# Optimization experiments

Measured on AMD Instinct MI355X. Metric: run time of the kernel, lower is better.

## Reference

```python
import jax, jax.numpy as jnp
import numpy as np

B, L, D_MODEL, H, D_K, D_V, C = 4, 2048, 512, 8, 64, 64, 5
LN_EPS = 1e-5


def setup_inputs() -> dict:
    key = jax.random.key(0)
    ks = jax.random.split(key, 9)
    u_k = min(int(C * np.log(L)), L)  # 38
    s = 1.0 / np.sqrt(D_MODEL)
    return {
        "input_Q": jax.random.normal(ks[0], (B, L, D_MODEL), jnp.float32),
        "input_K": jax.random.normal(ks[1], (B, L, D_MODEL), jnp.float32),
        "input_V": jax.random.normal(ks[2], (B, L, D_MODEL), jnp.float32),
        "W_Q": jax.random.normal(ks[3], (D_MODEL, H * D_K), jnp.float32) * s,
        "W_K": jax.random.normal(ks[4], (D_MODEL, H * D_K), jnp.float32) * s,
        "W_V": jax.random.normal(ks[5], (D_MODEL, H * D_V), jnp.float32) * s,
        "W_fc": jax.random.normal(ks[6], (H * D_V, D_MODEL), jnp.float32) * (1.0 / np.sqrt(H * D_V)),
        "ln_gamma": jnp.ones((D_MODEL,), jnp.float32),
        "ln_beta": jnp.zeros((D_MODEL,), jnp.float32),
        "index_sample": jax.random.randint(ks[7], (L, u_k), 0, L, jnp.int32),
    }


def reference(input_Q, input_K, input_V, W_Q, W_K, W_V, W_fc, ln_gamma, ln_beta, index_sample):
    Bb, L_Q, _ = input_Q.shape
    L_K = input_K.shape[1]
    u_q = min(int(C * np.log(L_Q)), L_Q)  # n_top queries kept

    # projections -> (B, H, L, d)
    Q = (input_Q @ W_Q).reshape(Bb, L_Q, H, D_K).transpose(0, 2, 1, 3)
    K = (input_K @ W_K).reshape(Bb, L_K, H, D_K).transpose(0, 2, 1, 3)
    V = (input_V @ W_V).reshape(Bb, L_K, H, D_V).transpose(0, 2, 1, 3)

    # sampled QK scores: gather u_k random keys per query position
    K_sample = K[:, :, index_sample, :]                      # (B,H,L_Q,u_k,d_k)
    QK_sample = jnp.einsum('bhqe,bhqke->bhqk', Q, K_sample)  # (B,H,L_Q,u_k)

    # sparsity measure M = max - mean, top-u_q queries
    M = QK_sample.max(axis=-1) - QK_sample.mean(axis=-1)     # (B,H,L_Q)
    _, idx = jax.lax.top_k(M, u_q)                           # (B,H,u_q)

    # attention only for selected queries
    Q_sel = jnp.take_along_axis(Q, idx[..., None], axis=2)   # (B,H,u_q,d_k)
    scores = jnp.einsum('bhue,bhke->bhuk', Q_sel, K) / np.sqrt(D_K)
    attn = jax.nn.softmax(scores, axis=-1)
    values = jnp.einsum('bhuk,bhkd->bhud', attn, V)          # (B,H,u_q,d_v)

    # initial context = mean of V (attn_mask is None), scatter selected rows
    context = jnp.broadcast_to(V.mean(axis=2, keepdims=True), (Bb, H, L_Q, D_V))
    bb = jnp.arange(Bb)[:, None, None]
    hh = jnp.arange(H)[None, :, None]
    context = context.at[bb, hh, idx].set(values)

    context = context.transpose(0, 2, 1, 3).reshape(Bb, L_Q, H * D_V)
    out = context @ W_fc                                     # dropout p=0.0

    y = out + input_Q
    mu = y.mean(axis=-1, keepdims=True)
    var = jnp.mean(jnp.square(y - mu), axis=-1, keepdims=True)
    y = (y - mu) / jnp.sqrt(var + LN_EPS) * ln_gamma + ln_beta
    return y, idx
```

## Files before the change

kernel.cpp:

```cpp
#include <hip/hip_runtime.h>
#include <hip/hip_bf16.h>

#define NB 4
#define NL 2048
#define NH 8
#define NDM 512
#define ND 64
#define KSPLIT 8
#define QB 8

typedef __attribute__((ext_vector_type(8))) short short8b;
typedef __attribute__((ext_vector_type(4))) float f32x4;

__global__ void wconv(const float* __restrict__ W, unsigned short* __restrict__ WT) {
  const int g = blockIdx.x * 256 + threadIdx.x;
  const int k = g >> 9, c = g & 511;
  __hip_bfloat16 hb = __float2bfloat16(W[(size_t)k * 512 + c]);
  WT[(size_t)c * 512 + k] = *reinterpret_cast<unsigned short*>(&hb);
}

__global__ void vmean_colmean(const float* __restrict__ inV, float* __restrict__ parts) {
  const int b = blockIdx.x, seg = blockIdx.y, t = threadIdx.x;
  const float* p = inV + ((size_t)b * NL + seg * 32) * NDM;
  float s0 = 0.f, s1 = 0.f;
  for (int r = 0; r < 32; ++r) {
    s0 += p[(size_t)r * NDM + t];
    s1 += p[(size_t)r * NDM + 256 + t];
  }
  parts[((size_t)b * 64 + seg) * NDM + t] = s0;
  parts[((size_t)b * 64 + seg) * NDM + 256 + t] = s1;
}
__global__ void vmean_gemm(const float* __restrict__ parts, const float* __restrict__ Wv,
                           float* __restrict__ Vm) {
  __shared__ float cm[512];
  const int b = blockIdx.x, t = threadIdx.x;
  float a0 = 0.f, a1 = 0.f;
  for (int g = 0; g < 64; ++g) {
    a0 += parts[((size_t)b * 64 + g) * NDM + t];
    a1 += parts[((size_t)b * 64 + g) * NDM + 256 + t];
  }
  cm[t] = a0 * (1.f / 2048.f);
  cm[t + 256] = a1 * (1.f / 2048.f);
  __syncthreads();
  const int c0 = blockIdx.y * 256 + t;
  float acc = 0.f;
  for (int k = 0; k < 512; ++k) acc += cm[k] * Wv[(size_t)k * NDM + c0];
  Vm[b * 512 + c0] = acc;
}

__global__ __launch_bounds__(256, 4) void proj3(
    const float* __restrict__ AQ, const float* __restrict__ AK,
    const float* __restrict__ wQm, const float* __restrict__ wKm,
    int gh0, float* __restrict__ Qc, float* __restrict__ Kc) {
  __shared__ float As_[32 * 132];
  __shared__ float Ws_[32 * 68];
  const int tid = threadIdx.x;
  const int bm = blockIdx.x;
  const int hl = blockIdx.y;
  const int mat = blockIdx.z;
  const int bh = gh0 + hl;
  const int b = bh >> 3, h = bh & 7;
  const float* A = (mat == 0) ? AQ : AK;
  const float* W = (mat == 0) ? wQm : wKm;
  float* D = (mat == 0) ? Qc : Kc;
  const float* Ab = A + (size_t)b * NL * NDM;
  const int colbase = h * 64;
  const int tm = tid >> 4, tn = tid & 15;
  float acc[8][4] = {};
  for (int k0 = 0; k0 < 512; k0 += 32) {
#pragma unroll
    for (int i = 0; i < 4; ++i) {
      int s = tid + i * 256;
      int r = s >> 3, c4 = (s & 7) * 4;
      float4 v = *reinterpret_cast<const float4*>(Ab + (size_t)(bm * 128 + r) * 512 + k0 + c4);
      As_[(c4 + 0) * 132 + r] = v.x;
      As_[(c4 + 1) * 132 + r] = v.y;
      As_[(c4 + 2) * 132 + r] = v.z;
      As_[(c4 + 3) * 132 + r] = v.w;
    }
#pragma unroll
    for (int i = 0; i < 2; ++i) {
      int s = tid + i * 256;
      int r = s >> 4, c4 = (s & 15) * 4;
      *reinterpret_cast<float4*>(&Ws_[r * 68 + c4]) =
          *reinterpret_cast<const float4*>(W + (size_t)(k0 + r) * 512 + colbase + c4);
    }
    __syncthreads();
#pragma unroll
    for (int kk = 0; kk < 32; ++kk) {
      float4 a0 = *reinterpret_cast<const float4*>(&As_[kk * 132 + tm * 4]);
      float4 a1 = *reinterpret_cast<const float4*>(&As_[kk * 132 + 64 + tm * 4]);
      float4 w  = *reinterpret_cast<const float4*>(&Ws_[kk * 68 + tn * 4]);
      float a[8] = {a0.x, a0.y, a0.z, a0.w, a1.x, a1.y, a1.z, a1.w};
      float wv[4] = {w.x, w.y, w.z, w.w};
#pragma unroll
      for (int ii = 0; ii < 8; ++ii)
#pragma unroll
        for (int jj = 0; jj < 4; ++jj) acc[ii][jj] += a[ii] * wv[jj];
    }
    __syncthreads();
  }
#pragma unroll
  for (int ii = 0; ii < 8; ++ii) {
    int row = bm * 128 + ((ii < 4) ? (tm * 4 + ii) : (64 + tm * 4 + (ii - 4)));
    float4 v = make_float4(acc[ii][0], acc[ii][1], acc[ii][2], acc[ii][3]);
    *reinterpret_cast<float4*>(D + ((size_t)hl * NL + row) * ND + tn * 4) = v;
  }
}

__global__ __launch_bounds__(256) void projV_mfma(
    const float* __restrict__ AV, const unsigned short* __restrict__ WT,
    int gh0, float* __restrict__ Vc) {
  const int wv = threadIdx.x >> 6, l = threadIdx.x & 63;
  const int bm = blockIdx.x;
  const int hl = blockIdx.y;
  const int bh = gh0 + hl;
  const int b = bh >> 3, h = bh & 7;
  const float* Ab = AV + (size_t)b * NL * NDM;
  const int row = bm * 64 + wv * 16 + (l & 15);
  const int kg = (l >> 4) * 8;
  f32x4 acc0 = {}, acc1 = {}, acc2 = {}, acc3 = {};
  for (int k0 = 0; k0 < 512; k0 += 32) {
    const float* ap = Ab + (size_t)row * 512 + k0 + kg;
    short8b af;
#pragma unroll
    for (int j = 0; j < 8; ++j) {
      __hip_bfloat16 hb = __float2bfloat16(ap[j]);
      af[j] = *reinterpret_cast<short*>(&hb);
    }
    const unsigned short* wp = WT + (size_t)(h * 64 + (l & 15)) * 512 + k0 + kg;
    short8b b0 = *reinterpret_cast<const short8b*>(wp);
    short8b b1 = *reinterpret_cast<const short8b*>(wp + 16 * 512);
    short8b b2 = *reinterpret_cast<const short8b*>(wp + 32 * 512);
    short8b b3 = *reinterpret_cast<const short8b*>(wp + 48 * 512);
    acc0 = __builtin_amdgcn_mfma_f32_16x16x32_bf16(af, b0, acc0, 0, 0, 0);
    acc1 = __builtin_amdgcn_mfma_f32_16x16x32_bf16(af, b1, acc1, 0, 0, 0);
    acc2 = __builtin_amdgcn_mfma_f32_16x16x32_bf16(af, b2, acc2, 0, 0, 0);
    acc3 = __builtin_amdgcn_mfma_f32_16x16x32_bf16(af, b3, acc3, 0, 0, 0);
  }
  const int rbase = bm * 64 + wv * 16 + (l >> 4) * 4;
  const int col = l & 15;
#pragma unroll
  for (int j = 0; j < 4; ++j) {
    size_t o = ((size_t)hl * NL + rbase + j) * ND + col;
    Vc[o] = acc0[j];
    Vc[o + 16] = acc1[j];
    Vc[o + 32] = acc2[j];
    Vc[o + 48] = acc3[j];
  }
}

template <int UK>
__global__ __launch_bounds__(256) void sample_scores_t(
    const float* __restrict__ Q, const float* __restrict__ K,
    const int* __restrict__ sampP, float* __restrict__ M) {
  __shared__ float KsAll[4][UK * 66];
  __shared__ float QsAll[4][68];
  const int wv = threadIdx.x >> 6, l = threadIdx.x & 63;
  const int gq = blockIdx.x * 4 + wv;
  const int hl = gq >> 11;
  const int q = gq & 2047;
  float* Ks = KsAll[wv];
  float* Qs = QsAll[wv];
  const float* Kb = K + (size_t)hl * NL * ND;
  Qs[l] = Q[(size_t)gq * ND + l];
  const int base = __builtin_amdgcn_readfirstlane(q) * UK;
#pragma unroll
  for (int r = 0; r < UK; ++r) {
    int kk = sampP[base + r] & (NL - 1);
    Ks[r * 66 + l] = Kb[(size_t)kk * ND + l];
  }
  __syncthreads();
  const int myk = (l < UK) ? l : (UK - 1);
  float acc = 0.f;
#pragma unroll
  for (int j = 0; j < 32; ++j) {
    float2 kv = *reinterpret_cast<const float2*>(&Ks[myk * 66 + 2 * j]);
    float2 qv = *reinterpret_cast<const float2*>(&Qs[2 * j]);
    acc += kv.x * qv.x + kv.y * qv.y;
  }
  float mval = (l < UK) ? acc : -1e30f;
  float sval = (l < UK) ? acc : 0.f;
#pragma unroll
  for (int o = 32; o; o >>= 1) {
    mval = fmaxf(mval, __shfl_xor(mval, o, 64));
    sval += __shfl_xor(sval, o, 64);
  }
  if (l == 0) M[gq] = mval - sval * (1.f / (float)UK);
}

__global__ void sample_scores_gen(const float* __restrict__ Q, const float* __restrict__ K,
                                  const int* __restrict__ sampP, float* __restrict__ M, int uk) {
  const int wave = threadIdx.x >> 6, lane = threadIdx.x & 63;
  const int gq = blockIdx.x * 4 + wave;
  const int hl = gq >> 11;
  const int q = gq & 2047;
  const float qv = Q[(size_t)gq * ND + lane];
  const float* Kbase = K + (size_t)hl * NL * ND;
  float mx = -1e30f, sm = 0.f;
  for (int k = 0; k < uk; ++k) {
    int kidx = sampP[q * uk + k] & (NL - 1);
    float p = qv * Kbase[(size_t)kidx * ND + lane];
#pragma unroll
    for (int o = 32; o; o >>= 1) p += __shfl_xor(p, o, 64);
    mx = fmaxf(mx, p);
    sm += p;
  }
  if (lane == 0) M[gq] = mx - sm / (float)uk;
}

__global__ void topk_kernel(const float* __restrict__ M, int* __restrict__ idxo,
                            float* __restrict__ outIdx, int uq) {
  __shared__ float mv[2048];
  __shared__ float bwv[4];
  __shared__ int bwi[4];
  const int bh = blockIdx.x, t = threadIdx.x;
  for (int i = 0; i < 8; ++i) mv[t + i * 256] = M[(size_t)bh * 2048 + t + i * 256];
  __syncthreads();
  for (int it = 0; it < uq; ++it) {
    float best = -1e38f; int bidx = 1 << 30;
#pragma unroll
    for (int i = 0; i < 8; ++i) {
      int id = t + i * 256;
      float v = mv[id];
      if (v > best || (v == best && id < bidx)) { best = v; bidx = id; }
    }
#pragma unroll
    for (int o = 32; o; o >>= 1) {
      float ov = __shfl_xor(best, o, 64);
      int oi = __shfl_xor(bidx, o, 64);
      if (ov > best || (ov == best && oi < bidx)) { best = ov; bidx = oi; }
    }
    if ((t & 63) == 0) { bwv[t >> 6] = best; bwi[t >> 6] = bidx; }
    __syncthreads();
    if (t == 0) {
      float bb = bwv[0]; int bi2 = bwi[0];
#pragma unroll
      for (int w = 1; w < 4; ++w) {
        if (bwv[w] > bb || (bwv[w] == bb && bwi[w] < bi2)) { bb = bwv[w]; bi2 = bwi[w]; }
      }
      int sel = bi2 & (NL - 1);
      idxo[bh * uq + it] = sel;
      outIdx[bh * uq + it] = (float)sel;
      mv[sel] = -1e38f;
    }
    __syncthreads();
  }
}

__global__ __launch_bounds__(256) void attn_part(
    const float* __restrict__ Qw, const float* __restrict__ Kw, const float* __restrict__ Vw,
    const int* __restrict__ idxo, float* __restrict__ pacc, float* __restrict__ pml, int uq) {
  __shared__ float Qs[QB][68];
  __shared__ float Ks[64][68];
  __shared__ float Vs[64][68];
  __shared__ float sc[QB][66];
  __shared__ float accs[QB][68];
  const int hl = blockIdx.x, qg = blockIdx.y, ks = blockIdx.z;
  const int t = threadIdx.x;
#pragma unroll
  for (int i = 0; i < 2; ++i) {
    int s = t + i * 256;
    int q = s >> 6, d = s & 63;
    int u = qg * QB + q;
    float v = 0.f;
    if (u < uq) {
      int qi = idxo[hl * uq + u] & (NL - 1);
      v = Qw[((size_t)hl * NL + qi) * ND + d];
    }
    Qs[q][d] = v;
    accs[q][d] = 0.f;
  }
  float m_run = -1e30f, l_run = 0.f;
  const int q2 = t >> 5, ln = t & 31;
  __syncthreads();
  const int kbeg = ks * (NL / KSPLIT);
  for (int k0 = kbeg; k0 < kbeg + NL / KSPLIT; k0 += 64) {
#pragma unroll
    for (int i = 0; i < 4; ++i) {
      int s = t + i * 256;
      int r = s >> 4, c4 = (s & 15) * 4;
      *reinterpret_cast<float4*>(&Ks[r][c4]) =
          *reinterpret_cast<const float4*>(Kw + ((size_t)hl * NL + k0 + r) * ND + c4);
      *reinterpret_cast<float4*>(&Vs[r][c4]) =
          *reinterpret_cast<const float4*>(Vw + ((size_t)hl * NL + k0 + r) * ND + c4);
    }
    __syncthreads();
    {
      const int q = t & 7, kk = t >> 3;
      float d0 = 0.f, d1 = 0.f;
#pragma unroll
      for (int dd = 0; dd < 64; dd += 4) {
        float4 qv = *reinterpret_cast<const float4*>(&Qs[q][dd]);
        float4 ka = *reinterpret_cast<const float4*>(&Ks[kk][dd]);
        float4 kb = *reinterpret_cast<const float4*>(&Ks[kk + 32][dd]);
        d0 += qv.x * ka.x + qv.y * ka.y + qv.z * ka.z + qv.w * ka.w;
        d1 += qv.x * kb.x + qv.y * kb.y + qv.z * kb.z + qv.w * kb.w;
      }
      sc[q][kk] = d0 * 0.125f;
      sc[q][kk + 32] = d1 * 0.125f;
    }
    __syncthreads();
    {
      float s0 = sc[q2][ln], s1 = sc[q2][ln + 32];
      float tmax = fmaxf(s0, s1);
#pragma unroll
      for (int o = 16; o; o >>= 1) tmax = fmaxf(tmax, __shfl_xor(tmax, o, 64));
      float mnew = fmaxf(m_run, tmax);
      float scl = __expf(m_run - mnew);
      float p0 = __expf(s0 - mnew), p1 = __expf(s1 - mnew);
      float tsum = p0 + p1;
#pragma unroll
      for (int o = 16; o; o >>= 1) tsum += __shfl_xor(tsum, o, 64);
      l_run = l_run * scl + tsum;
      m_run = mnew;
      sc[q2][ln] = p0; sc[q2][ln + 32] = p1;
      float a0 = accs[q2][2 * ln] * scl, a1 = accs[q2][2 * ln + 1] * scl;
#pragma unroll 8
      for (int k = 0; k < 64; ++k) {
        float p = sc[q2][k];
        a0 += p * Vs[k][2 * ln];
        a1 += p * Vs[k][2 * ln + 1];
      }
      accs[q2][2 * ln] = a0; accs[q2][2 * ln + 1] = a1;
    }
    __syncthreads();
  }
  const int u = qg * QB + q2;
  if (u < uq) {
    size_t g = ((size_t)hl * uq + u) * KSPLIT + ks;
    pacc[g * ND + 2 * ln] = accs[q2][2 * ln];
    pacc[g * ND + 2 * ln + 1] = accs[q2][2 * ln + 1];
    if (ln == 0) { pml[g * 2] = m_run; pml[g * 2 + 1] = l_run; }
  }
}

__global__ void attn_merge(const float* __restrict__ pacc, const float* __restrict__ pml,
                           float* __restrict__ vals, int uq) {
  const int g = blockIdx.x;
  const int d = threadIdx.x;
  float mstar = -1e30f;
#pragma unroll
  for (int s = 0; s < KSPLIT; ++s) mstar = fmaxf(mstar, pml[((size_t)g * KSPLIT + s) * 2]);
  float num = 0.f, den = 0.f;
#pragma unroll
  for (int s = 0; s < KSPLIT; ++s) {
    float e = __expf(pml[((size_t)g * KSPLIT + s) * 2] - mstar);
    den += e * pml[((size_t)g * KSPLIT + s) * 2 + 1];
    num += e * pacc[((size_t)g * KSPLIT + s) * ND + d];
  }
  vals[(size_t)g * ND + d] = num / den;
}

__global__ void selmap_init(short* __restrict__ selmap) {
  const int g = blockIdx.x * 256 + threadIdx.x;
  selmap[g] = -1;
  selmap[g + 32768] = -1;
}
__global__ void selmap_fill(const int* __restrict__ idxo, short* __restrict__ selmap, int uq) {
  const int g = blockIdx.x * 256 + threadIdx.x;
  if (g >= NB * NH * uq) return;
  const int bh = g / uq, u = g - bh * uq;
  const int b = bh >> 3, h = bh & 7;
  const int l = idxo[g] & (NL - 1);
  selmap[((size_t)b * NL + l) * NH + h] = (short)u;
}

__global__ void base_gemm(const float* __restrict__ Vm, const float* __restrict__ Wfc,
                          float* __restrict__ base) {
  __shared__ float vm[512];
  const int b = blockIdx.x, t = threadIdx.x;
  vm[t] = Vm[b * 512 + t];
  vm[t + 256] = Vm[b * 512 + t + 256];
  __syncthreads();
  const int c0 = blockIdx.y * 256 + t;
  float acc = 0.f;
  for (int k = 0; k < 512; ++k) acc += vm[k] * Wfc[(size_t)k * 512 + c0];
  base[b * 512 + c0] = acc;
}

__global__ void corr_gemm(const float* __restrict__ vals, const float* __restrict__ Vm,
                          const float* __restrict__ Wfc, float* __restrict__ corr, int uq) {
  __shared__ float diff[64];
  const int g = blockIdx.x, t = threadIdx.x;
  const int bh = g / uq;
  const int h = bh & 7;
  if (t < 64) diff[t] = vals[(size_t)g * 64 + t] - Vm[bh * 64 + t];
  __syncthreads();
  float a0 = 0.f, a1 = 0.f;
#pragma unroll
  for (int d = 0; d < 64; ++d) {
    a0 += diff[d] * Wfc[(size_t)(h * 64 + d) * 512 + t];
    a1 += diff[d] * Wfc[(size_t)(h * 64 + d) * 512 + t + 256];
  }
  corr[(size_t)g * 512 + t] = a0;
  corr[(size_t)g * 512 + t + 256] = a1;
}

__global__ void ln_fused(const float* __restrict__ base, const float* __restrict__ resid,
                         const float* __restrict__ corr, const short* __restrict__ selmap,
                         const float* __restrict__ gamma, const float* __restrict__ beta,
                         float* __restrict__ out, int uq) {
  __shared__ float red[256];
  const int row = blockIdx.x, t = threadIdx.x;
  const int b = row >> 11;
  float y0 = base[b * 512 + t] + resid[(size_t)row * 512 + t];
  float y1 = base[b * 512 + 256 + t] + resid[(size_t)row * 512 + 256 + t];
#pragma unroll
  for (int h = 0; h < NH; ++h) {
    int s = selmap[(size_t)row * NH + h];
    if (s >= 0 && s < uq) {
      const float* cp = corr + (size_t)((b * NH + h) * uq + s) * 512;
      y0 += cp[t];
      y1 += cp[t + 256];
    }
  }
  red[t] = y0 + y1;
  __syncthreads();
  for (int s = 128; s; s >>= 1) { if (t < s) red[t] += red[t + s]; __syncthreads(); }
  const float mu = red[0] * (1.f / 512.f);
  __syncthreads();
  const float d0 = y0 - mu, d1 = y1 - mu;
  red[t] = d0 * d0 + d1 * d1;
  __syncthreads();
  for (int s = 128; s; s >>= 1) { if (t < s) red[t] += red[t + s]; __syncthreads(); }
  const float rs = rsqrtf(red[0] * (1.f / 512.f) + 1e-5f);
  __syncthreads();
  out[(size_t)row * 512 + t] = d0 * rs * gamma[t] + beta[t];
  out[(size_t)row * 512 + 256 + t] = d1 * rs * gamma[256 + t] + beta[256 + t];
}

extern "C" void kernel_launch(void* const* d_in, const int* in_sizes, int n_in,
                              void* d_out, int out_size, void* d_ws, size_t ws_size,
                              hipStream_t stream) {
  const float* inQ = (const float*)d_in[0];
  const float* inK = (const float*)d_in[1];
  const float* inV = (const float*)d_in[2];
  const float* wQ = (const float*)d_in[3];
  const float* wK = (const float*)d_in[4];
  const float* wV = (const float*)d_in[5];
  const float* wFC = (const float*)d_in[6];
  const float* gamma = (const float*)d_in[7];
  const float* beta = (const float*)d_in[8];
  const int* samp = (const int*)d_in[9];

  const int nsamp = in_sizes[9];
  const int uk = nsamp / NL;
  const int uq = uk;
  const int nqg = (uq + QB - 1) / QB;

  if (out_size < NB * NL * NDM + NB * NH * uq) return;

  const size_t perH = 3 * 131072 + 2048 + (size_t)uq * KSPLIT * 64 + (size_t)uq * KSPLIT * 2;
  const size_t fixed = (size_t)32 * uq * 64 + 2048 + 2048 + (size_t)32 * uq * 512
                     + (size_t)32 * uq + 32768 + 131072 + 131072 + 256;
  int hcg = 0;
  for (int c = 32; c >= 1; c >>= 1) {
    if ((perH * (size_t)c + fixed + 256) * 4ull <= ws_size) { hcg = c; break; }
  }
  if (hcg == 0) return;

  float* ws = (float*)d_ws;
  float* Qc = ws;
  float* Kc = Qc + (size_t)hcg * 131072;
  float* Vc = Kc + (size_t)hcg * 131072;
  float* Mb = Vc + (size_t)hcg * 131072;
  float* pacc = Mb + (size_t)hcg * 2048;
  float* pml = pacc + (size_t)hcg * uq * KSPLIT * 64;
  float* vals = pml + (size_t)hcg * uq * KSPLIT * 2;
  float* Vm = vals + (size_t)32 * uq * 64;
  float* base = Vm + 2048;
  float* corr = base + 2048;
  int* idxo = (int*)(corr + (size_t)32 * uq * 512);
  short* selmap = (short*)(idxo + (size_t)32 * uq);
  unsigned short* WTv = (unsigned short*)(selmap + 65536);
  float* vparts = (float*)(WTv + 262144);

  float* out = (float*)d_out;
  float* outIdx = out + (size_t)NB * NL * NDM;

  wconv<<<1024, 256, 0, stream>>>(wV, WTv);
  vmean_colmean<<<dim3(NB, 64), 256, 0, stream>>>(inV, vparts);
  vmean_gemm<<<dim3(NB, 2), 256, 0, stream>>>(vparts, wV, Vm);

  for (int gh0 = 0; gh0 < NB * NH; gh0 += hcg) {
    proj3<<<dim3(16, hcg, 2), 256, 0, stream>>>(inQ, inK, wQ, wK, gh0, Qc, Kc);
    projV_mfma<<<dim3(32, hcg), 256, 0, stream>>>(inV, WTv, gh0, Vc);
    if (uk == 38)
      sample_scores_t<38><<<hcg * NL / 4, 256, 0, stream>>>(Qc, Kc, samp, Mb);
    else
      sample_scores_gen<<<hcg * NL / 4, 256, 0, stream>>>(Qc, Kc, samp, Mb, uk);
    topk_kernel<<<hcg, 256, 0, stream>>>(Mb, idxo + (size_t)gh0 * uq,
                                         outIdx + (size_t)gh0 * uq, uq);
    attn_part<<<dim3(hcg, nqg, KSPLIT), 256, 0, stream>>>(Qc, Kc, Vc,
                                                          idxo + (size_t)gh0 * uq,
                                                          pacc, pml, uq);
    attn_merge<<<hcg * uq, 64, 0, stream>>>(pacc, pml, vals + (size_t)gh0 * uq * ND, uq);
  }

  selmap_init<<<NB * NL * NH / 2 / 256, 256, 0, stream>>>(selmap);
  selmap_fill<<<(NB * NH * uq + 255) / 256, 256, 0, stream>>>(idxo, selmap, uq);
  base_gemm<<<dim3(NB, 2), 256, 0, stream>>>(Vm, wFC, base);
  corr_gemm<<<NB * NH * uq, 256, 0, stream>>>(vals, Vm, wFC, corr, uq);
  ln_fused<<<NB * NL, 256, 0, stream>>>(base, inQ, corr, selmap, gamma, beta, out, uq);
}
```

Before: 361.4 us.

## Cache per-thread top-k maxima, fuse selmap fill into top-k, double K split

Top-k now keeps a per-thread running maximum and rescans only in the single thread that owned the selected element, so each iteration no longer rescans all 2048 values across every thread. The selection map is written directly inside the top-k kernel and initialised with a memset, which removes two small kernel launches. KSPLIT is raised from 8 to 16 to give the partial-attention kernel more blocks, at the cost of a larger merge step. The pml/pacc buffer sizing depends on KSPLIT and must still fit the workspace.

Measured after the change: 363.3 us, median of 2. No clear change (+0.5%).

```diff
diff --git a/kernel.cpp b/kernel.cpp
--- a/kernel.cpp
+++ b/kernel.cpp
@@ -6,7 +6,7 @@
 #define NH 8
 #define NDM 512
 #define ND 64
-#define KSPLIT 8
+#define KSPLIT 16
 #define QB 8
 
 typedef __attribute__((ext_vector_type(8))) short short8b;
@@ -210,39 +210,53 @@
 }
 
 __global__ void topk_kernel(const float* __restrict__ M, int* __restrict__ idxo,
-                            float* __restrict__ outIdx, int uq) {
+                            float* __restrict__ outIdx, short* __restrict__ selmap,
+                            int gh0, int uq) {
   __shared__ float mv[2048];
   __shared__ float bwv[4];
   __shared__ int bwi[4];
   const int bh = blockIdx.x, t = threadIdx.x;
-  for (int i = 0; i < 8; ++i) mv[t + i * 256] = M[(size_t)bh * 2048 + t + i * 256];
+  const int bhg = gh0 + bh;
+  const int bb = bhg >> 3, hh = bhg & 7;
+  float lv = -1e38f; int li = 1 << 30;
+#pragma unroll
+  for (int i = 0; i < 8; ++i) {
+    int id = t + i * 256;
+    float v = M[(size_t)bh * 2048 + id];
+    mv[id] = v;
+    if (v > lv || (v == lv && id < li)) { lv = v; li = id; }
+  }
   __syncthreads();
   for (int it = 0; it < uq; ++it) {
-    float best = -1e38f; int bidx = 1 << 30;
-#pragma unroll
-    for (int i = 0; i < 8; ++i) {
-      int id = t + i * 256;
-      float v = mv[id];
-      if (v > best || (v == best && id < bidx)) { best = v; bidx = id; }
-    }
+    float bv = lv; int bi = li;
 #pragma unroll
     for (int o = 32; o; o >>= 1) {
-      float ov = __shfl_xor(best, o, 64);
-      int oi = __shfl_xor(bidx, o, 64);
-      if (ov > best || (ov == best && oi < bidx)) { best = ov; bidx = oi; }
-    }
-    if ((t & 63) == 0) { bwv[t >> 6] = best; bwi[t >> 6] = bidx; }
-    __syncthreads();
+      float ov = __shfl_xor(bv, o, 64);
+      int oi = __shfl_xor(bi, o, 64);
+      if (ov > bv || (ov == bv && oi < bi)) { bv = ov; bi = oi; }
+    }
+    if ((t & 63) == 0) { bwv[t >> 6] = bv; bwi[t >> 6] = bi; }
+    __syncthreads();
+    float gb = bwv[0]; int gi = bwi[0];
+#pragma unroll
+    for (int w = 1; w < 4; ++w) {
+      if (bwv[w] > gb || (bwv[w] == gb && bwi[w] < gi)) { gb = bwv[w]; gi = bwi[w]; }
+    }
+    const int sel = gi & (NL - 1);
     if (t == 0) {
-      float bb = bwv[0]; int bi2 = bwi[0];
-#pragma unroll
-      for (int w = 1; w < 4; ++w) {
-        if (bwv[w] > bb || (bwv[w] == bb && bwi[w] < bi2)) { bb = bwv[w]; bi2 = bwi[w]; }
-      }
-      int sel = bi2 & (NL - 1);
       idxo[bh * uq + it] = sel;
       outIdx[bh * uq + it] = (float)sel;
+      selmap[((size_t)bb * NL + sel) * NH + hh] = (short)it;
+    }
+    if ((sel & 255) == t) {
       mv[sel] = -1e38f;
+      lv = -1e38f; li = 1 << 30;
+#pragma unroll
+      for (int i = 0; i < 8; ++i) {
+        int id = t + i * 256;
+        float v = mv[id];
+        if (v > lv || (v == lv && id < li)) { lv = v; li = id; }
+      }
     }
     __syncthreads();
   }
@@ -350,20 +364,6 @@
     num += e * pacc[((size_t)g * KSPLIT + s) * ND + d];
   }
   vals[(size_t)g * ND + d] = num / den;
-}
-
-__global__ void selmap_init(short* __restrict__ selmap) {
-  const int g = blockIdx.x * 256 + threadIdx.x;
-  selmap[g] = -1;
-  selmap[g + 32768] = -1;
-}
-__global__ void selmap_fill(const int* __restrict__ idxo, short* __restrict__ selmap, int uq) {
-  const int g = blockIdx.x * 256 + threadIdx.x;
-  if (g >= NB * NH * uq) return;
-  const int bh = g / uq, u = g - bh * uq;
-  const int b = bh >> 3, h = bh & 7;
-  const int l = idxo[g] & (NL - 1);
-  selmap[((size_t)b * NL + l) * NH + h] = (short)u;
 }
 
 __global__ void base_gemm(const float* __restrict__ Vm, const float* __restrict__ Wfc,
@@ -482,6 +482,7 @@
   wconv<<<1024, 256, 0, stream>>>(wV, WTv);
   vmean_colmean<<<dim3(NB, 64), 256, 0, stream>>>(inV, vparts);
   vmean_gemm<<<dim3(NB, 2), 256, 0, stream>>>(vparts, wV, Vm);
+  hipMemsetAsync(selmap, 0xFF, (size_t)NB * NL * NH * sizeof(short), stream);
 
   for (int gh0 = 0; gh0 < NB * NH; gh0 += hcg) {
     proj3<<<dim3(16, hcg, 2), 256, 0, stream>>>(inQ, inK, wQ, wK, gh0, Qc, Kc);
@@ -491,15 +492,13 @@
     else
       sample_scores_gen<<<hcg * NL / 4, 256, 0, stream>>>(Qc, Kc, samp, Mb, uk);
     topk_kernel<<<hcg, 256, 0, stream>>>(Mb, idxo + (size_t)gh0 * uq,
-                                         outIdx + (size_t)gh0 * uq, uq);
+                                         outIdx + (size_t)gh0 * uq, selmap, gh0, uq);
     attn_part<<<dim3(hcg, nqg, KSPLIT), 256, 0, stream>>>(Qc, Kc, Vc,
                                                           idxo + (size_t)gh0 * uq,
                                                           pacc, pml, uq);
     attn_merge<<<hcg * uq, 64, 0, stream>>>(pacc, pml, vals + (size_t)gh0 * uq * ND, uq);
   }
 
-  selmap_init<<<NB * NL * NH / 2 / 256, 256, 0, stream>>>(selmap);
-  selmap_fill<<<(NB * NH * uq + 255) / 256, 256, 0, stream>>>(idxo, selmap, uq);
   base_gemm<<<dim3(NB, 2), 256, 0, stream>>>(Vm, wFC, base);
   corr_gemm<<<NB * NH * uq, 256, 0, stream>>>(vals, Vm, wFC, corr, uq);
   ln_fused<<<NB * NL, 256, 0, stream>>>(base, inQ, corr, selmap, gamma, beta, out, uq);
```
